# Kernel optimization log

Measured on AMD Instinct MI355X. Metric: run time of the kernel, lower is better.

Reference implementation:

```python
import jax, jax.numpy as jnp
import numpy as np
import math

N_NODES = 100000
N_EDGES = 1600000
IN_FEATS = 128
H_FEATS = 64
NUM_CLASSES = 2
D = 2  # num_layers -> d+1 = 3 filters, each polynomial of degree d


def _calc_thetas(d):
    # Beta-Bernstein polynomial coefficients, ascending powers of x.
    # f_i(x) = (x/2)^i (1-x/2)^(d-i) / B(i+1, d+1-i),  B = i!(d-i)!/(d+1)!
    thetas = []
    for i in range(d + 1):
        beta = math.factorial(i) * math.factorial(d - i) / math.factorial(d + 1)
        p = np.array([1.0])
        for _ in range(i):
            p = np.convolve(p, [0.0, 0.5])
        for _ in range(d - i):
            p = np.convolve(p, [1.0, -0.5])
        thetas.append([float(c) for c in (p / beta)])
    return thetas

THETAS = _calc_thetas(D)


def setup_inputs() -> dict:
    key = jax.random.key(0)
    ks = jax.random.split(key, 12)
    x = jax.random.normal(ks[0], (N_NODES, IN_FEATS), dtype=jnp.float32)
    edge_index = jax.random.randint(ks[1], (2, N_EDGES), 0, N_NODES, dtype=jnp.int64)
    s = 0.05
    W1 = jax.random.normal(ks[2], (IN_FEATS, H_FEATS), jnp.float32) * s
    b1 = jnp.zeros((H_FEATS,), jnp.float32)
    W2 = jax.random.normal(ks[3], (H_FEATS, H_FEATS), jnp.float32) * s
    b2 = jnp.zeros((H_FEATS,), jnp.float32)
    Wm1 = jax.random.normal(ks[4], (H_FEATS * len(THETAS), H_FEATS), jnp.float32) * s
    bm1 = jnp.zeros((H_FEATS,), jnp.float32)
    Wm2 = jax.random.normal(ks[5], (H_FEATS, NUM_CLASSES), jnp.float32) * s
    bm2 = jnp.zeros((NUM_CLASSES,), jnp.float32)
    return {"x": x, "edge_index": edge_index, "W1": W1, "b1": b1,
            "W2": W2, "b2": b2, "Wm1": Wm1, "bm1": bm1, "Wm2": Wm2, "bm2": bm2}


def reference(x, edge_index, W1, b1, W2, b2, Wm1, bm1, Wm2, bm2):
    N = x.shape[0]
    src, dst = edge_index[0], edge_index[1]
    # in-degrees (edges point src -> dst, message summed at dst)
    deg = jax.ops.segment_sum(jnp.ones((edge_index.shape[1],), x.dtype), dst,
                              num_segments=N)
    dinv = jnp.clip(deg, 1.0, None) ** -0.5  # [N]
    dinv = dinv[:, None]
    # two linear + ReLU layers
    h = jax.nn.relu(x @ W1 + b1)
    h = jax.nn.relu(h @ W2 + b2)
    # PolyConv per theta: feat <- feat - D^-1/2 A D^-1/2 feat; acc += theta_k feat
    outs = []
    for theta in THETAS:
        feat = h
        acc = theta[0] * feat
        for k in range(1, len(theta)):
            msg = jax.ops.segment_sum((feat * dinv)[src], dst, num_segments=N)
            feat = feat - msg * dinv
            acc = acc + theta[k] * feat
        outs.append(acc)
    h_final = jnp.concatenate(outs, axis=-1)  # [N, h_feats*(d+1)]
    # MLP (2 layers): Linear -> ReLU -> Linear
    h_final = jax.nn.relu(h_final @ Wm1 + bm1)
    return h_final @ Wm2 + bm2
```

## Files before the change

### kernel.cpp

```cpp
#include <hip/hip_runtime.h>
#include <math.h>

#define N_NODES 100000
#define N_EDGES 1600000
#define IN_F 128
#define H_F 64

#define NBKT 391
#define BSEG 5120
#define BCAP 5120

#define NP        100096
#define OFF_CNT   0
#define OFF_MPK   512
#define OFF_W1H   6656
#define OFF_W1L   10752
#define OFF_W2H   14848
#define OFF_W2L   16896
#define OFF_OFFS  18944
#define OFF_D2    (OFF_OFFS + NP + 64)
#define OFF_RD    (OFF_D2 + NP)
#define OFF_DINV  (OFF_RD + NP)
#define OFF_ADJ   (OFF_DINV + NP)
#define OFF_H0    (OFF_ADJ + N_EDGES)
#define OFF_H1    (OFF_H0 + N_NODES*32)
#define OFF_H2    (OFF_H1 + N_NODES*32)

typedef __attribute__((ext_vector_type(8))) short bf16x8;
typedef __attribute__((ext_vector_type(4))) float f32x4;

__device__ __forceinline__ unsigned short bf16rn(float f) {
    unsigned u = __float_as_uint(f);
    u += 0x7FFFu + ((u >> 16) & 1u);
    return (unsigned short)(u >> 16);
}
#define UNPK(u, lo, hi) { lo = __uint_as_float((u) << 16); hi = __uint_as_float((u) & 0xFFFF0000u); }
#define ACC8(v) { float l, h; \
    UNPK(v.x, l, h); a0 += l; a1 += h; \
    UNPK(v.y, l, h); a2 += l; a3 += h; \
    UNPK(v.z, l, h); a4 += l; a5 += h; \
    UNPK(v.w, l, h); a6 += l; a7 += h; }

__global__ __launch_bounds__(256) void k_prep(const float* __restrict__ Wm1,
        const float* __restrict__ W1, const float* __restrict__ W2,
        unsigned short* __restrict__ mpk,
        unsigned short* __restrict__ w1h, unsigned short* __restrict__ w1l,
        unsigned short* __restrict__ w2h, unsigned short* __restrict__ w2l,
        int* __restrict__ cnt) {
    int idx = blockIdx.x * 256 + threadIdx.x;
    if (idx < 512) cnt[idx] = 0;
    if (idx < 12288) {
        int j = idx & 7;
        int n = (idx >> 3) & 63;
        int qd = (idx >> 9) & 3;
        int s = idx >> 11;
        int k = s * 32 + qd * 8 + j;
        int p = k >> 6;
        int kk = k & 63;
        float w0 = Wm1[kk * 64 + n];
        float w1 = Wm1[(64 + kk) * 64 + n];
        float w2 = Wm1[(128 + kk) * 64 + n];
        float v;
        if (p == 0)      v = 3.0f * w0;
        else if (p == 1) v = 3.0f * (w1 - w0);
        else             v = 0.75f * (w0 + w2) - 1.5f * w1;
        mpk[idx] = bf16rn(v);
    } else if (idx < 12288 + 8192) {
        int lin = idx - 12288;
        int j = lin & 7, cc = (lin >> 3) & 15, ot = (lin >> 7) & 3;
        int qd = (lin >> 9) & 3, ks = lin >> 11;
        float v = W1[(ks * 32 + qd * 8 + j) * 64 + ot * 16 + cc];
        unsigned short h = bf16rn(v);
        w1h[lin] = h;
        w1l[lin] = bf16rn(v - __uint_as_float((unsigned)h << 16));
    } else if (idx < 24576) {
        int lin = idx - 20480;
        int j = lin & 7, cc = (lin >> 3) & 15, ot = (lin >> 7) & 3;
        int qd = (lin >> 9) & 3, ks = lin >> 11;
        float v = W2[(ks * 32 + qd * 8 + j) * 64 + ot * 16 + cc];
        unsigned short h = bf16rn(v);
        w2h[lin] = h;
        w2l[lin] = bf16rn(v - __uint_as_float((unsigned)h << 16));
    }
}

__global__ __launch_bounds__(256) void k_bin(const int* __restrict__ src,
        const int* __restrict__ dst, int* __restrict__ cnt,
        int* __restrict__ binned, int E) {
    __shared__ int hist[4][NBKT + 1];
    __shared__ int cur4[4][NBKT + 1];
    int t = threadIdx.x;
    int w = t >> 6;
    for (int i = t; i < 4 * (NBKT + 1); i += 256) (&hist[0][0])[i] = 0;
    __syncthreads();
    int base = blockIdx.x * 8192 + t;
    int d[32];
    #pragma unroll
    for (int i = 0; i < 32; ++i) {
        int e = base + i * 256;
        int dd = (e < E) ? dst[e] : -1;
        d[i] = dd;
        if (dd >= 0) atomicAdd(&hist[w][dd >> 8], 1);
    }
    __syncthreads();
    for (int i = t; i < NBKT; i += 256) {
        int h0 = hist[0][i], h1 = hist[1][i], h2 = hist[2][i], h3 = hist[3][i];
        int tot = h0 + h1 + h2 + h3;
        int b0 = (tot > 0) ? atomicAdd(&cnt[i], tot) : 0;
        cur4[0][i] = b0;
        cur4[1][i] = b0 + h0;
        cur4[2][i] = b0 + h0 + h1;
        cur4[3][i] = b0 + h0 + h1 + h2;
    }
    __syncthreads();
    #pragma unroll
    for (int i = 0; i < 32; ++i) {
        int e = base + i * 256;
        if (e < E) {
            int s = src[e];
            int dd = d[i];
            int b = dd >> 8;
            int p = atomicAdd(&cur4[w][b], 1);
            if (p < BSEG) binned[b * BSEG + p] = ((dd & 255) << 17) | s;
        }
    }
}

__global__ __launch_bounds__(256) void k_cfill(const int* __restrict__ binned,
        const int* __restrict__ cnt, int* __restrict__ offs, int* __restrict__ adj,
        float* __restrict__ d2a, float* __restrict__ rda, float* __restrict__ dinva) {
    __shared__ int csum[256];
    __shared__ int degl[256];
    __shared__ int curl[256];
    __shared__ int wsum[4];
    __shared__ int adjl[BCAP];
    int b = blockIdx.x, t = threadIdx.x;
    int p = 0;
    if (2 * t < NBKT) p += cnt[2 * t];
    if (2 * t + 1 < NBKT) p += cnt[2 * t + 1];
    csum[t] = p;
    __syncthreads();
    #pragma unroll
    for (int off = 1; off < 256; off <<= 1) {
        int u = (t >= off) ? csum[t - off] : 0;
        __syncthreads();
        csum[t] += u;
        __syncthreads();
    }
    int b2 = b >> 1;
    int baseb = ((b2 > 0) ? csum[b2 - 1] : 0) + ((b & 1) ? cnt[b - 1] : 0);
    int cntb = cnt[b];
    if (b == 0 && t == 0) offs[N_NODES] = N_EDGES;
    int n0 = b << 8;
    const int* bp = binned + b * BSEG;
    degl[t] = 0;
    __syncthreads();
    for (int i = t; i < cntb; i += 256) atomicAdd(&degl[bp[i] >> 17], 1);
    __syncthreads();
    int d0 = degl[t];
    int lane = t & 63, wid = t >> 6;
    int inc = d0;
    #pragma unroll
    for (int off = 1; off < 64; off <<= 1) {
        int v = __shfl_up(inc, off, 64);
        if (lane >= off) inc += v;
    }
    if (lane == 63) wsum[wid] = inc;
    __syncthreads();
    int wb = 0;
    for (int w = 0; w < wid; ++w) wb += wsum[w];
    int excl = wb + inc - d0;
    curl[t] = excl;
    int n = n0 + t;
    if (n < N_NODES) {
        offs[n] = baseb + excl;
        float df = (float)d0;
        if (df < 1.f) df = 1.f;
        float di = 1.0f / sqrtf(df);
        dinva[n] = di;
        d2a[n] = di * di;
        rda[n] = sqrtf(df);
    }
    __syncthreads();
    for (int i = t; i < cntb; i += 256) {
        int w = bp[i];
        int loc = w >> 17;
        int s = w & 0x1FFFF;
        int pp = atomicAdd(&curl[loc], 1);
        if (pp < BCAP) adjl[pp] = s;
        else adj[baseb + pp] = s;
    }
    __syncthreads();
    int lim = cntb < BCAP ? cntb : BCAP;
    for (int i = t; i < lim; i += 256) adj[baseb + i] = adjl[i];
}

__global__ __launch_bounds__(256) void k_gemm12(const float* __restrict__ x,
        const unsigned short* __restrict__ w1h, const unsigned short* __restrict__ w1l,
        const unsigned short* __restrict__ w2h, const unsigned short* __restrict__ w2l,
        const float* __restrict__ b1, const float* __restrict__ b2,
        const float* __restrict__ dinva, unsigned short* __restrict__ gsh, int N) {
    __shared__ unsigned int Hl[4][16 * 65];
    __shared__ unsigned short Sl[4][16 * 66];
    int t = threadIdx.x;
    int w = t >> 6, lane = t & 63;
    int c = lane & 15, qd = lane >> 4;
    int nbase = blockIdx.x * 64 + w * 16;
    if (nbase >= N) return;
    int node = nbase + c;
    int nclamp = (node < N) ? node : N - 1;

    f32x4 a0 = {0.f,0.f,0.f,0.f}, a1 = a0, a2 = a0, a3 = a0;
    #pragma unroll
    for (int ks = 0; ks < 4; ++ks) {
        const float* xp = x + (size_t)nclamp * IN_F + ks * 32 + qd * 8;
        float4 xa = *(const float4*)xp;
        float4 xb = *(const float4*)(xp + 4);
        float xs[8] = {xa.x, xa.y, xa.z, xa.w, xb.x, xb.y, xb.z, xb.w};
        bf16x8 ahi, alo;
        #pragma unroll
        for (int j = 0; j < 8; ++j) {
            unsigned short h = bf16rn(xs[j]);
            ahi[j] = (short)h;
            alo[j] = (short)bf16rn(xs[j] - __uint_as_float((unsigned)h << 16));
        }
        const unsigned short* bh = w1h + (size_t)(ks * 4 + qd) * 512;
        const unsigned short* bl = w1l + (size_t)(ks * 4 + qd) * 512;
        bf16x8 h0 = *(const bf16x8*)(bh + 0 * 128 + c * 8);
        bf16x8 l0 = *(const bf16x8*)(bl + 0 * 128 + c * 8);
        bf16x8 h1 = *(const bf16x8*)(bh + 1 * 128 + c * 8);
        bf16x8 l1 = *(const bf16x8*)(bl + 1 * 128 + c * 8);
        bf16x8 h2 = *(const bf16x8*)(bh + 2 * 128 + c * 8);
        bf16x8 l2 = *(const bf16x8*)(bl + 2 * 128 + c * 8);
        bf16x8 h3 = *(const bf16x8*)(bh + 3 * 128 + c * 8);
        bf16x8 l3 = *(const bf16x8*)(bl + 3 * 128 + c * 8);
        a0 = __builtin_amdgcn_mfma_f32_16x16x32_bf16(ahi, h0, a0, 0, 0, 0);
        a1 = __builtin_amdgcn_mfma_f32_16x16x32_bf16(ahi, h1, a1, 0, 0, 0);
        a2 = __builtin_amdgcn_mfma_f32_16x16x32_bf16(ahi, h2, a2, 0, 0, 0);
        a3 = __builtin_amdgcn_mfma_f32_16x16x32_bf16(ahi, h3, a3, 0, 0, 0);
        a0 = __builtin_amdgcn_mfma_f32_16x16x32_bf16(alo, h0, a0, 0, 0, 0);
        a1 = __builtin_amdgcn_mfma_f32_16x16x32_bf16(alo, h1, a1, 0, 0, 0);
        a2 = __builtin_amdgcn_mfma_f32_16x16x32_bf16(alo, h2, a2, 0, 0, 0);
        a3 = __builtin_amdgcn_mfma_f32_16x16x32_bf16(alo, h3, a3, 0, 0, 0);
        a0 = __builtin_amdgcn_mfma_f32_16x16x32_bf16(ahi, l0, a0, 0, 0, 0);
        a1 = __builtin_amdgcn_mfma_f32_16x16x32_bf16(ahi, l1, a1, 0, 0, 0);
        a2 = __builtin_amdgcn_mfma_f32_16x16x32_bf16(ahi, l2, a2, 0, 0, 0);
        a3 = __builtin_amdgcn_mfma_f32_16x16x32_bf16(ahi, l3, a3, 0, 0, 0);
    }
    #pragma unroll
    for (int ot = 0; ot < 4; ++ot) {
        float bb = b1[ot * 16 + c];
        f32x4 a = (ot == 0) ? a0 : (ot == 1) ? a1 : (ot == 2) ? a2 : a3;
        #pragma unroll
        for (int r = 0; r < 4; ++r) {
            float h = fmaxf(a[r] + bb, 0.f);
            unsigned short hh = bf16rn(h);
            unsigned short hl = bf16rn(h - __uint_as_float((unsigned)hh << 16));
            Hl[w][(qd * 4 + r) * 65 + ot * 16 + c] = ((unsigned)hh << 16) | hl;
        }
    }
    f32x4 d0 = {0.f,0.f,0.f,0.f}, d1 = d0, d2 = d0, d3 = d0;
    #pragma unroll
    for (int ks = 0; ks < 2; ++ks) {
        bf16x8 ahi, alo;
        #pragma unroll
        for (int j = 0; j < 8; ++j) {
            unsigned v = Hl[w][c * 65 + ks * 32 + qd * 8 + j];
            ahi[j] = (short)(v >> 16);
            alo[j] = (short)(v & 0xFFFFu);
        }
        const unsigned short* bh = w2h + (size_t)(ks * 4 + qd) * 512;
        const unsigned short* bl = w2l + (size_t)(ks * 4 + qd) * 512;
        bf16x8 h0 = *(const bf16x8*)(bh + 0 * 128 + c * 8);
        bf16x8 l0 = *(const bf16x8*)(bl + 0 * 128 + c * 8);
        bf16x8 h1 = *(const bf16x8*)(bh + 1 * 128 + c * 8);
        bf16x8 l1 = *(const bf16x8*)(bl + 1 * 128 + c * 8);
        bf16x8 h2 = *(const bf16x8*)(bh + 2 * 128 + c * 8);
        bf16x8 l2 = *(const bf16x8*)(bl + 2 * 128 + c * 8);
        bf16x8 h3 = *(const bf16x8*)(bh + 3 * 128 + c * 8);
        bf16x8 l3 = *(const bf16x8*)(bl + 3 * 128 + c * 8);
        d0 = __builtin_amdgcn_mfma_f32_16x16x32_bf16(ahi, h0, d0, 0, 0, 0);
        d1 = __builtin_amdgcn_mfma_f32_16x16x32_bf16(ahi, h1, d1, 0, 0, 0);
        d2 = __builtin_amdgcn_mfma_f32_16x16x32_bf16(ahi, h2, d2, 0, 0, 0);
        d3 = __builtin_amdgcn_mfma_f32_16x16x32_bf16(ahi, h3, d3, 0, 0, 0);
        d0 = __builtin_amdgcn_mfma_f32_16x16x32_bf16(alo, h0, d0, 0, 0, 0);
        d1 = __builtin_amdgcn_mfma_f32_16x16x32_bf16(alo, h1, d1, 0, 0, 0);
        d2 = __builtin_amdgcn_mfma_f32_16x16x32_bf16(alo, h2, d2, 0, 0, 0);
        d3 = __builtin_amdgcn_mfma_f32_16x16x32_bf16(alo, h3, d3, 0, 0, 0);
        d0 = __builtin_amdgcn_mfma_f32_16x16x32_bf16(ahi, l0, d0, 0, 0, 0);
        d1 = __builtin_amdgcn_mfma_f32_16x16x32_bf16(ahi, l1, d1, 0, 0, 0);
        d2 = __builtin_amdgcn_mfma_f32_16x16x32_bf16(ahi, l2, d2, 0, 0, 0);
        d3 = __builtin_amdgcn_mfma_f32_16x16x32_bf16(ahi, l3, d3, 0, 0, 0);
    }
    #pragma unroll
    for (int ot = 0; ot < 4; ++ot) {
        float bb = b2[ot * 16 + c];
        f32x4 a = (ot == 0) ? d0 : (ot == 1) ? d1 : (ot == 2) ? d2 : d3;
        #pragma unroll
        for (int r = 0; r < 4; ++r) {
            int nd = nbase + qd * 4 + r;
            float di = dinva[(nd < N) ? nd : N - 1];
            Sl[w][(qd * 4 + r) * 66 + ot * 16 + c] = bf16rn(di * fmaxf(a[r] + bb, 0.f));
        }
    }
    #pragma unroll
    for (int i = 0; i < 4; ++i) {
        int nl = i * 4 + qd;
        int nd = nbase + nl;
        if (nd < N) {
            ushort4 v;
            v.x = Sl[w][nl * 66 + c * 4 + 0];
            v.y = Sl[w][nl * 66 + c * 4 + 1];
            v.z = Sl[w][nl * 66 + c * 4 + 2];
            v.w = Sl[w][nl * 66 + c * 4 + 3];
            *(ushort4*)(gsh + (size_t)nd * 64 + c * 4) = v;
        }
    }
}

__global__ __launch_bounds__(256) void k_prop(const unsigned short* __restrict__ gh,
        unsigned short* __restrict__ gout, const int* __restrict__ offs,
        const int* __restrict__ adj, const float* __restrict__ d2a, int N) {
    int t = threadIdx.x;
    int lane = t & 63;
    int g = lane >> 3;
    int q = lane & 7;
    int n = blockIdx.x * 4 + (t >> 6);
    if (n >= N) return;
    int beg = offs[n], end = offs[n + 1];
    float d2n = d2a[n];
    uint4 sv = *(const uint4*)(gh + (size_t)n * 64 + 8 * q);
    float a0 = 0.f, a1 = 0.f, a2 = 0.f, a3 = 0.f;
    float a4 = 0.f, a5 = 0.f, a6 = 0.f, a7 = 0.f;
    int e0 = beg + g;
    int e1 = e0 + 8;
    bool p0 = e0 < end;
    bool p1 = e1 < end;
    uint4 v0, v1;
    if (p0) v0 = *(const uint4*)(gh + (size_t)adj[e0] * 64 + 8 * q);
    if (p1) v1 = *(const uint4*)(gh + (size_t)adj[e1] * 64 + 8 * q);
    int e = e1 + 8;
    while (p1) {
        ACC8(v0);
        v0 = v1;
        p1 = e < end;
        if (p1) v1 = *(const uint4*)(gh + (size_t)adj[e] * 64 + 8 * q);
        e += 8;
    }
    if (p0) ACC8(v0);
    #pragma unroll
    for (int m = 8; m < 64; m <<= 1) {
        a0 += __shfl_xor(a0, m); a1 += __shfl_xor(a1, m);
        a2 += __shfl_xor(a2, m); a3 += __shfl_xor(a3, m);
        a4 += __shfl_xor(a4, m); a5 += __shfl_xor(a5, m);
        a6 += __shfl_xor(a6, m); a7 += __shfl_xor(a7, m);
    }
    if (g == 0) {
        float l, h;
        uint4 r;
        UNPK(sv.x, l, h);
        r.x = ((unsigned)bf16rn(fmaf(-d2n, a1, h)) << 16) | bf16rn(fmaf(-d2n, a0, l));
        UNPK(sv.y, l, h);
        r.y = ((unsigned)bf16rn(fmaf(-d2n, a3, h)) << 16) | bf16rn(fmaf(-d2n, a2, l));
        UNPK(sv.z, l, h);
        r.z = ((unsigned)bf16rn(fmaf(-d2n, a5, h)) << 16) | bf16rn(fmaf(-d2n, a4, l));
        UNPK(sv.w, l, h);
        r.w = ((unsigned)bf16rn(fmaf(-d2n, a7, h)) << 16) | bf16rn(fmaf(-d2n, a6, l));
        *(uint4*)(gout + (size_t)n * 64 + 8 * q) = r;
    }
}

__global__ __launch_bounds__(256) void k_final(const unsigned short* __restrict__ g0h,
        const unsigned short* __restrict__ g1h, const unsigned short* __restrict__ g2h,
        const unsigned short* __restrict__ mpk, const float* __restrict__ bm1,
        const float* __restrict__ Wm2, const float* __restrict__ bm2,
        const float* __restrict__ rda, float* __restrict__ out, int N) {
    int t = threadIdx.x;
    int w = t >> 6, lane = t & 63;
    int c = lane & 15, qd = lane >> 4;
    int nbase = blockIdx.x * 64 + w * 16;
    if (nbase >= N) return;
    int node = nbase + c;
    int nclamp = (node < N) ? node : N - 1;
    const unsigned short* bufs[3] = {g0h, g1h, g2h};
    f32x4 acc0 = {0.f, 0.f, 0.f, 0.f};
    f32x4 acc1 = {0.f, 0.f, 0.f, 0.f};
    f32x4 acc2 = {0.f, 0.f, 0.f, 0.f};
    f32x4 acc3 = {0.f, 0.f, 0.f, 0.f};
    #pragma unroll
    for (int s = 0; s < 6; ++s) {
        const unsigned short* gp = bufs[s >> 1];
        int k0 = (s & 1) * 32;
        bf16x8 a = *(const bf16x8*)(gp + (size_t)nclamp * 64 + k0 + qd * 8);
        const unsigned short* mb = mpk + (size_t)((s * 4 + qd) * 64) * 8;
        bf16x8 b0 = *(const bf16x8*)(mb + (size_t)(c) * 8);
        bf16x8 b1 = *(const bf16x8*)(mb + (size_t)(16 + c) * 8);
        bf16x8 b2 = *(const bf16x8*)(mb + (size_t)(32 + c) * 8);
        bf16x8 b3 = *(const bf16x8*)(mb + (size_t)(48 + c) * 8);
        acc0 = __builtin_amdgcn_mfma_f32_16x16x32_bf16(a, b0, acc0, 0, 0, 0);
        acc1 = __builtin_amdgcn_mfma_f32_16x16x32_bf16(a, b1, acc1, 0, 0, 0);
        acc2 = __builtin_amdgcn_mfma_f32_16x16x32_bf16(a, b2, acc2, 0, 0, 0);
        acc3 = __builtin_amdgcn_mfma_f32_16x16x32_bf16(a, b3, acc3, 0, 0, 0);
    }
    float rdr[4];
    #pragma unroll
    for (int r = 0; r < 4; ++r) {
        int nd = nbase + qd * 4 + r;
        rdr[r] = rda[(nd < N) ? nd : N - 1];
    }
    float p0[4] = {0.f, 0.f, 0.f, 0.f};
    float p1[4] = {0.f, 0.f, 0.f, 0.f};
    #pragma unroll
    for (int ot = 0; ot < 4; ++ot) {
        int col = ot * 16 + c;
        float bmc = bm1[col];
        float wc0 = Wm2[col * 2 + 0];
        float wc1 = Wm2[col * 2 + 1];
        f32x4 a = (ot == 0) ? acc0 : (ot == 1) ? acc1 : (ot == 2) ? acc2 : acc3;
        #pragma unroll
        for (int r = 0; r < 4; ++r) {
            float h = fmaxf(fmaf(rdr[r], a[r], bmc), 0.f);
            p0[r] = fmaf(h, wc0, p0[r]);
            p1[r] = fmaf(h, wc1, p1[r]);
        }
    }
    #pragma unroll
    for (int m = 1; m < 16; m <<= 1) {
        #pragma unroll
        for (int r = 0; r < 4; ++r) {
            p0[r] += __shfl_xor(p0[r], m);
            p1[r] += __shfl_xor(p1[r], m);
        }
    }
    if (c == 0) {
        float bo0 = bm2[0], bo1 = bm2[1];
        #pragma unroll
        for (int r = 0; r < 4; ++r) {
            int nd = nbase + qd * 4 + r;
            if (nd < N) {
                float2 o;
                o.x = p0[r] + bo0;
                o.y = p1[r] + bo1;
                *(float2*)(out + (size_t)nd * 2) = o;
            }
        }
    }
}

extern "C" void kernel_launch(void* const* d_in, const int* in_sizes, int n_in,
                              void* d_out, int out_size, void* d_ws, size_t ws_size,
                              hipStream_t stream) {
    const float* x   = (const float*)d_in[0];
    const int*   ei  = (const int*)d_in[1];
    const float* W1  = (const float*)d_in[2];
    const float* b1  = (const float*)d_in[3];
    const float* W2  = (const float*)d_in[4];
    const float* b2  = (const float*)d_in[5];
    const float* Wm1 = (const float*)d_in[6];
    const float* bm1 = (const float*)d_in[7];
    const float* Wm2 = (const float*)d_in[8];
    const float* bm2 = (const float*)d_in[9];
    float* out = (float*)d_out;

    int* ws = (int*)d_ws;
    int*   cnt   = ws + OFF_CNT;
    unsigned short* mpk = (unsigned short*)(ws + OFF_MPK);
    unsigned short* w1h = (unsigned short*)(ws + OFF_W1H);
    unsigned short* w1l = (unsigned short*)(ws + OFF_W1L);
    unsigned short* w2h = (unsigned short*)(ws + OFF_W2H);
    unsigned short* w2l = (unsigned short*)(ws + OFF_W2L);
    int*   offs  = ws + OFF_OFFS;
    float* d2a   = (float*)(ws + OFF_D2);
    float* rda   = (float*)(ws + OFF_RD);
    float* dinva = (float*)(ws + OFF_DINV);
    int*   adj   = ws + OFF_ADJ;
    unsigned short* gs0h = (unsigned short*)(ws + OFF_H0);
    unsigned short* gs1h = (unsigned short*)(ws + OFF_H1);
    unsigned short* gs2h = (unsigned short*)(ws + OFF_H2);
    int*   binned = ws + OFF_H1;

    const int* srcp = ei;
    const int* dstp = ei + N_EDGES;

    k_prep<<<96, 256, 0, stream>>>(Wm1, W1, W2, mpk, w1h, w1l, w2h, w2l, cnt);
    k_bin<<<(N_EDGES + 8191) / 8192, 256, 0, stream>>>(srcp, dstp, cnt, binned, N_EDGES);
    k_cfill<<<NBKT, 256, 0, stream>>>(binned, cnt, offs, adj, d2a, rda, dinva);

    int nblk = (N_NODES + 63) / 64;
    k_gemm12<<<nblk, 256, 0, stream>>>(x, w1h, w1l, w2h, w2l, b1, b2, dinva, gs0h, N_NODES);

    k_prop<<<(N_NODES + 3) / 4, 256, 0, stream>>>(gs0h, gs1h, offs, adj, d2a, N_NODES);
    k_prop<<<(N_NODES + 3) / 4, 256, 0, stream>>>(gs1h, gs2h, offs, adj, d2a, N_NODES);

    k_final<<<nblk, 256, 0, stream>>>(gs0h, gs1h, gs2h, mpk, bm1, Wm2, bm2, rda, out, N_NODES);
}
```

Baseline: 249.3 us.

## Assign four nodes per wavefront in propagation and prescale adjacency to byte offsets

The propagation kernel now handles four destination nodes per 64-lane wavefront, 16 lanes each, instead of one node per wavefront with 8 edge groups. This cuts wasted lanes and cross-lane reductions for low-degree nodes (average degree 16) down to a single xor shuffle. Adjacency indices are stored pre-shifted by 7 so each gather address is a byte offset plus a lane offset. Accumulation uses packed float2 adds and the index load is software-pipelined one step ahead. The cost is fewer edges in flight per node, so high-degree nodes take longer and per-lane memory-level parallelism drops.

```diff
diff --git a/kernel.cpp b/kernel.cpp
--- a/kernel.cpp
+++ b/kernel.cpp
@@ -28,6 +28,7 @@
 
 typedef __attribute__((ext_vector_type(8))) short bf16x8;
 typedef __attribute__((ext_vector_type(4))) float f32x4;
+typedef __attribute__((ext_vector_type(2))) float f32x2;
 
 __device__ __forceinline__ unsigned short bf16rn(float f) {
     unsigned u = __float_as_uint(f);
@@ -35,11 +36,8 @@
     return (unsigned short)(u >> 16);
 }
 #define UNPK(u, lo, hi) { lo = __uint_as_float((u) << 16); hi = __uint_as_float((u) & 0xFFFF0000u); }
-#define ACC8(v) { float l, h; \
-    UNPK(v.x, l, h); a0 += l; a1 += h; \
-    UNPK(v.y, l, h); a2 += l; a3 += h; \
-    UNPK(v.z, l, h); a4 += l; a5 += h; \
-    UNPK(v.w, l, h); a6 += l; a7 += h; }
+#define ACC2(u, A) { f32x2 t_; t_.x = __uint_as_float((u) << 16); \
+                     t_.y = __uint_as_float((u) & 0xFFFF0000u); A += t_; }
 
 __global__ __launch_bounds__(256) void k_prep(const float* __restrict__ Wm1,
         const float* __restrict__ W1, const float* __restrict__ W2,
@@ -188,11 +186,11 @@
         int s = w & 0x1FFFF;
         int pp = atomicAdd(&curl[loc], 1);
         if (pp < BCAP) adjl[pp] = s;
-        else adj[baseb + pp] = s;
+        else adj[baseb + pp] = s << 7;
     }
     __syncthreads();
     int lim = cntb < BCAP ? cntb : BCAP;
-    for (int i = t; i < lim; i += 256) adj[baseb + i] = adjl[i];
+    for (int i = t; i < lim; i += 256) adj[baseb + i] = adjl[i] << 7;
 }
 
 __global__ __launch_bounds__(256) void k_gemm12(const float* __restrict__ x,
@@ -320,52 +318,56 @@
 
 __global__ __launch_bounds__(256) void k_prop(const unsigned short* __restrict__ gh,
         unsigned short* __restrict__ gout, const int* __restrict__ offs,
-        const int* __restrict__ adj, const float* __restrict__ d2a, int N) {
+        const int* __restrict__ adjb, const float* __restrict__ d2a, int N) {
     int t = threadIdx.x;
     int lane = t & 63;
-    int g = lane >> 3;
     int q = lane & 7;
-    int n = blockIdx.x * 4 + (t >> 6);
-    if (n >= N) return;
-    int beg = offs[n], end = offs[n + 1];
-    float d2n = d2a[n];
-    uint4 sv = *(const uint4*)(gh + (size_t)n * 64 + 8 * q);
-    float a0 = 0.f, a1 = 0.f, a2 = 0.f, a3 = 0.f;
-    float a4 = 0.f, a5 = 0.f, a6 = 0.f, a7 = 0.f;
-    int e0 = beg + g;
-    int e1 = e0 + 8;
-    bool p0 = e0 < end;
-    bool p1 = e1 < end;
+    int g = (lane >> 3) & 1;
+    int n = blockIdx.x * 16 + (t >> 6) * 4 + (lane >> 4);
+    int nc = (n < N) ? n : N - 1;
+    int beg = offs[nc], end = offs[nc + 1];
+    float d2n = d2a[nc];
+    const char* base = (const char*)gh;
+    uint4 sv = *(const uint4*)(gh + (size_t)nc * 64 + 8 * q);
+    f32x2 A0 = {0.f, 0.f}, A1 = A0, A2 = A0, A3 = A0;
+    unsigned qo = (unsigned)(q << 4);
+    int e = beg + g;
+    bool pa0 = e < end;
+    bool pa1 = e + 2 < end;
+    unsigned off0 = 0, off1 = 0;
+    if (pa0) off0 = (unsigned)adjb[e];
+    if (pa1) off1 = (unsigned)adjb[e + 2];
     uint4 v0, v1;
-    if (p0) v0 = *(const uint4*)(gh + (size_t)adj[e0] * 64 + 8 * q);
-    if (p1) v1 = *(const uint4*)(gh + (size_t)adj[e1] * 64 + 8 * q);
-    int e = e1 + 8;
-    while (p1) {
-        ACC8(v0);
+    if (pa0) v0 = *(const uint4*)(base + (size_t)(off0 + qo));
+    if (pa1) v1 = *(const uint4*)(base + (size_t)(off1 + qo));
+    int en = e + 4;
+    bool pv = pa1;
+    while (pv) {
+        bool pa2 = en < end;
+        unsigned off2 = 0;
+        if (pa2) off2 = (unsigned)adjb[en];
+        ACC2(v0.x, A0); ACC2(v0.y, A1); ACC2(v0.z, A2); ACC2(v0.w, A3);
         v0 = v1;
-        p1 = e < end;
-        if (p1) v1 = *(const uint4*)(gh + (size_t)adj[e] * 64 + 8 * q);
-        e += 8;
-    }
-    if (p0) ACC8(v0);
-    #pragma unroll
-    for (int m = 8; m < 64; m <<= 1) {
-        a0 += __shfl_xor(a0, m); a1 += __shfl_xor(a1, m);
-        a2 += __shfl_xor(a2, m); a3 += __shfl_xor(a3, m);
-        a4 += __shfl_xor(a4, m); a5 += __shfl_xor(a5, m);
-        a6 += __shfl_xor(a6, m); a7 += __shfl_xor(a7, m);
-    }
-    if (g == 0) {
+        pv = pa2;
+        if (pv) v1 = *(const uint4*)(base + (size_t)(off2 + qo));
+        en += 2;
+    }
+    if (pa0) { ACC2(v0.x, A0); ACC2(v0.y, A1); ACC2(v0.z, A2); ACC2(v0.w, A3); }
+    A0.x += __shfl_xor(A0.x, 8); A0.y += __shfl_xor(A0.y, 8);
+    A1.x += __shfl_xor(A1.x, 8); A1.y += __shfl_xor(A1.y, 8);
+    A2.x += __shfl_xor(A2.x, 8); A2.y += __shfl_xor(A2.y, 8);
+    A3.x += __shfl_xor(A3.x, 8); A3.y += __shfl_xor(A3.y, 8);
+    if (g == 0 && n < N) {
         float l, h;
         uint4 r;
         UNPK(sv.x, l, h);
-        r.x = ((unsigned)bf16rn(fmaf(-d2n, a1, h)) << 16) | bf16rn(fmaf(-d2n, a0, l));
+        r.x = ((unsigned)bf16rn(fmaf(-d2n, A0.y, h)) << 16) | bf16rn(fmaf(-d2n, A0.x, l));
         UNPK(sv.y, l, h);
-        r.y = ((unsigned)bf16rn(fmaf(-d2n, a3, h)) << 16) | bf16rn(fmaf(-d2n, a2, l));
+        r.y = ((unsigned)bf16rn(fmaf(-d2n, A1.y, h)) << 16) | bf16rn(fmaf(-d2n, A1.x, l));
         UNPK(sv.z, l, h);
-        r.z = ((unsigned)bf16rn(fmaf(-d2n, a5, h)) << 16) | bf16rn(fmaf(-d2n, a4, l));
+        r.z = ((unsigned)bf16rn(fmaf(-d2n, A2.y, h)) << 16) | bf16rn(fmaf(-d2n, A2.x, l));
         UNPK(sv.w, l, h);
-        r.w = ((unsigned)bf16rn(fmaf(-d2n, a7, h)) << 16) | bf16rn(fmaf(-d2n, a6, l));
+        r.w = ((unsigned)bf16rn(fmaf(-d2n, A3.y, h)) << 16) | bf16rn(fmaf(-d2n, A3.x, l));
         *(uint4*)(gout + (size_t)n * 64 + 8 * q) = r;
     }
 }
@@ -489,8 +491,8 @@
     int nblk = (N_NODES + 63) / 64;
     k_gemm12<<<nblk, 256, 0, stream>>>(x, w1h, w1l, w2h, w2l, b1, b2, dinva, gs0h, N_NODES);
 
-    k_prop<<<(N_NODES + 3) / 4, 256, 0, stream>>>(gs0h, gs1h, offs, adj, d2a, N_NODES);
-    k_prop<<<(N_NODES + 3) / 4, 256, 0, stream>>>(gs1h, gs2h, offs, adj, d2a, N_NODES);
+    k_prop<<<(N_NODES + 15) / 16, 256, 0, stream>>>(gs0h, gs1h, offs, adj, d2a, N_NODES);
+    k_prop<<<(N_NODES + 15) / 16, 256, 0, stream>>>(gs1h, gs2h, offs, adj, d2a, N_NODES);
 
     k_final<<<nblk, 256, 0, stream>>>(gs0h, gs1h, gs2h, mpk, bm1, Wm2, bm2, rda, out, N_NODES);
 }
```

After: 235.8 us, median of 2. 1.06x faster.
